# Kernel optimization log

Hardware: AMD Instinct MI355X
Metric: run time of the kernel (lower is better)

Reference implementation:

```python
import jax, jax.numpy as jnp
import numpy as np

N = 50000   # nodes
E = 600000  # directed edges (self-loops added inside reference, per GCNConv default)
G = 64      # graphs in the batch
D = 128     # in_features
H = 128     # hidden_channels
C = 10      # num_classes


def setup_inputs() -> dict:
    key = jax.random.key(0)
    ks = jax.random.split(key, 9)
    x = jax.random.normal(ks[0], (N, D), dtype=jnp.float32)
    edge_index = jax.random.randint(ks[1], (2, E), 0, N, dtype=jnp.int64)
    batch = jnp.sort(jax.random.randint(ks[2], (N,), 0, G, dtype=jnp.int64))
    # GCNConv weights (glorot-ish scale) and biases; final linear layer
    W1 = jax.random.normal(ks[3], (D, H), dtype=jnp.float32) / np.sqrt(D).astype(np.float32)
    b1 = jnp.zeros((H,), dtype=jnp.float32)
    W2 = jax.random.normal(ks[4], (H, H), dtype=jnp.float32) / np.sqrt(H).astype(np.float32)
    b2 = jnp.zeros((H,), dtype=jnp.float32)
    Wlin = jax.random.normal(ks[5], (H, C), dtype=jnp.float32) / np.sqrt(H).astype(np.float32)
    blin = jnp.zeros((C,), dtype=jnp.float32)
    return {"x": x, "W1": W1, "b1": b1, "W2": W2, "b2": b2,
            "Wlin": Wlin, "blin": blin, "edge_index": edge_index, "batch": batch}


def _gcn_conv(x, W, b, row, col, norm):
    # x' = D^{-1/2}(A+I)D^{-1/2} (x W) + b ; aggregate messages from row (src) into col (dst)
    h = x @ W                                   # [N, H] dense GEMM
    msg = norm[:, None] * h[row]                # gather by source index [E+N, H]
    out = jax.ops.segment_sum(msg, col, num_segments=N)  # scatter-add to targets
    return out + b


def reference(x, W1, b1, W2, b2, Wlin, blin, edge_index, batch):
    loops = jnp.arange(N, dtype=edge_index.dtype)
    row = jnp.concatenate([edge_index[0], loops])   # sources (+ self loops)
    col = jnp.concatenate([edge_index[1], loops])   # targets (+ self loops)
    # symmetric degree normalization (degrees >= 1 thanks to self loops)
    deg = jax.ops.segment_sum(jnp.ones_like(col, dtype=jnp.float32), col, num_segments=N)
    dinv = jax.lax.rsqrt(deg)
    norm = dinv[row] * dinv[col]                    # [E+N]

    h = jax.nn.relu(_gcn_conv(x, W1, b1, row, col, norm))
    h = _gcn_conv(h, W2, b2, row, col, norm)

    # global mean pool over graphs
    sums = jax.ops.segment_sum(h, batch, num_segments=G)                       # [G, H]
    cnt = jax.ops.segment_sum(jnp.ones((N,), dtype=jnp.float32), batch, num_segments=G)
    pooled = sums / jnp.maximum(cnt, 1.0)[:, None]

    return pooled @ Wlin + blin                     # logits [G, C]
```

## Files before the change

### kernel.cpp

```cpp
#include <hip/hip_runtime.h>

#define NN 50000
#define NE 600000
#define NG 64
#define DIM 128
#define NCLS 10
#define SB 196
#define NNP 50176
#define KBLK 224
#define KCH 224
#define CAP 64
#define E2B ((NE / 2 + 255) / 256)

typedef unsigned short ushort;
typedef __attribute__((ext_vector_type(8))) short short8;
typedef __attribute__((ext_vector_type(4))) float float4v;

__device__ __forceinline__ ushort f2bf(float f) {
    unsigned u = __float_as_uint(f);
    u += 0x7fff + ((u >> 16) & 1);
    return (ushort)(u >> 16);
}
__device__ __forceinline__ void acc8(float* a, uint4 v) {
    a[0] += __uint_as_float(v.x << 16); a[1] += __uint_as_float(v.x & 0xffff0000u);
    a[2] += __uint_as_float(v.y << 16); a[3] += __uint_as_float(v.y & 0xffff0000u);
    a[4] += __uint_as_float(v.z << 16); a[5] += __uint_as_float(v.z & 0xffff0000u);
    a[6] += __uint_as_float(v.w << 16); a[7] += __uint_as_float(v.w & 0xffff0000u);
}

__global__ void k_init(int* __restrict__ cnt, const float* __restrict__ W1,
                       ushort* __restrict__ Wsw, float* __restrict__ Wd) {
    int b = blockIdx.x, t = threadIdx.x;
    if (b < SB) {
        int i = b * 256 + t;
        if (i < NN) cnt[i] = 0;
    } else if (b < SB + 64) {
        int tid = (b - SB) * 256 + t;
        int j = tid & 7;
        int lane = (tid >> 3) & 63;
        int frag = tid >> 9;
        int nt = frag >> 2, kc = frag & 3;
        int k = kc * 32 + (lane >> 4) * 8 + j;
        int n = nt * 16 + (lane & 15);
        Wsw[tid] = f2bf(W1[k * DIM + n]);
    } else {
        float4* w4 = (float4*)Wd;
        int base = (b - SB - 64) * 256 + t;
#pragma unroll
        for (int i = 0; i < 4; ++i)
            w4[base + i * 200704] = make_float4(0.f, 0.f, 0.f, 0.f);
    }
}

__global__ void k_fill(const int* __restrict__ row, const int* __restrict__ col,
                       int* __restrict__ cnt, int* __restrict__ ell) {
    int e = (blockIdx.x * blockDim.x + threadIdx.x) * 2;
    if (e < NE) {
        int2 r = *(const int2*)(row + e);
        int2 c = *(const int2*)(col + e);
        int p0 = atomicAdd(&cnt[c.x], 1);
        if (p0 < CAP) ell[c.x * CAP + p0] = r.x;
        int p1 = atomicAdd(&cnt[c.y], 1);
        if (p1 < CAP) ell[c.y * CAP + p1] = r.y;
    }
}

__global__ void k_pd(const int* __restrict__ cnt, const int* __restrict__ batch,
                     float* __restrict__ dinv, int2* __restrict__ pdat) {
    int i = blockIdx.x * 256 + threadIdx.x;
    if (i < NN) {
        float d = rsqrtf(1.0f + (float)cnt[i]);
        dinv[i] = d;
        pdat[i] = make_int2(batch[i], __float_as_int(d));
    }
}

__global__ void k_wbuild(const int* __restrict__ row, const int* __restrict__ col,
                         const int2* __restrict__ pdat, const float* __restrict__ dinv,
                         float* __restrict__ Wd) {
    int b = blockIdx.x, t = threadIdx.x;
    if (b < E2B) {
        int e = (b * 256 + t) * 2;
        if (e < NE) {
            int2 r = *(const int2*)(row + e);
            int2 c = *(const int2*)(col + e);
            int2 p0 = pdat[c.x];
            int2 p1 = pdat[c.y];
            atomicAdd(&Wd[(size_t)p0.x * NNP + r.x], __int_as_float(p0.y) * dinv[r.x]);
            atomicAdd(&Wd[(size_t)p1.x * NNP + r.y], __int_as_float(p1.y) * dinv[r.y]);
        }
    } else {
        int n = (b - E2B) * 256 + t;
        if (n < NN) {
            int2 p = pdat[n];
            float d = __int_as_float(p.y);
            atomicAdd(&Wd[(size_t)p.x * NNP + n], d * d);
        }
    }
}

__global__ __launch_bounds__(256) void k_gemm_mfma(const float* __restrict__ Ain,
                                                   const ushort* __restrict__ Wsw,
                                                   const float* __restrict__ dinv,
                                                   ushort* __restrict__ Hs) {
    const int t = threadIdx.x;
    const int wave = t >> 6, lane = t & 63;
    const int m = lane & 15, quad = lane >> 4;
    const int row0 = blockIdx.x * 64 + wave * 16;

    short8 bfrag[8][4];
#pragma unroll
    for (int nt = 0; nt < 8; ++nt)
#pragma unroll
        for (int kc = 0; kc < 4; ++kc)
            bfrag[nt][kc] = *(const short8*)(Wsw + ((nt * 4 + kc) * 64 + lane) * 8);

    float4v acc[8];
#pragma unroll
    for (int nt = 0; nt < 8; ++nt) acc[nt] = (float4v){0.f, 0.f, 0.f, 0.f};

    const int row = row0 + m;
    const int rclamp = row < NN ? row : NN - 1;

#pragma unroll
    for (int kc = 0; kc < 4; ++kc) {
        const float* ap = Ain + (size_t)rclamp * DIM + kc * 32 + quad * 8;
        float4 v0 = *(const float4*)ap;
        float4 v1 = *(const float4*)(ap + 4);
        union { short8 v; ushort u[8]; } tmp;
        tmp.u[0] = f2bf(v0.x); tmp.u[1] = f2bf(v0.y);
        tmp.u[2] = f2bf(v0.z); tmp.u[3] = f2bf(v0.w);
        tmp.u[4] = f2bf(v1.x); tmp.u[5] = f2bf(v1.y);
        tmp.u[6] = f2bf(v1.z); tmp.u[7] = f2bf(v1.w);
        short8 a = tmp.v;
#pragma unroll
        for (int nt = 0; nt < 8; ++nt)
            acc[nt] = __builtin_amdgcn_mfma_f32_16x16x32_bf16(a, bfrag[nt][kc], acc[nt], 0, 0, 0);
    }

#pragma unroll
    for (int reg = 0; reg < 4; ++reg) {
        int r = row0 + quad * 4 + reg;
        if (r < NN) {
            float d = dinv[r];
#pragma unroll
            for (int nt = 0; nt < 8; ++nt)
                Hs[(size_t)r * DIM + nt * 16 + m] = f2bf(d * acc[nt][reg]);
        }
    }
}

__global__ __launch_bounds__(256) void k_gather_ell(const int* __restrict__ ell,
                                                    const int* __restrict__ deg,
                                                    const float* __restrict__ dinv,
                                                    const float* __restrict__ bias,
                                                    const ushort* __restrict__ Hs,
                                                    ushort* __restrict__ out) {
    int gt = blockIdx.x * blockDim.x + threadIdx.x;
    int node = gt >> 4, lane = gt & 15;
    if (node >= NN) return;
    const int* rowp = ell + node * CAP;
    int end = min(deg[node], CAP);
    const size_t off = (size_t)lane * 8;

    float a[8] = {0.f, 0.f, 0.f, 0.f, 0.f, 0.f, 0.f, 0.f};
    acc8(a, *(const uint4*)(Hs + (size_t)node * DIM + off));

    int e = 0;
    for (; e + 8 <= end; e += 8) {
        int r0 = rowp[e], r1 = rowp[e + 1], r2 = rowp[e + 2], r3 = rowp[e + 3];
        int r4 = rowp[e + 4], r5 = rowp[e + 5], r6 = rowp[e + 6], r7 = rowp[e + 7];
        uint4 v0 = *(const uint4*)(Hs + (size_t)r0 * DIM + off);
        uint4 v1 = *(const uint4*)(Hs + (size_t)r1 * DIM + off);
        uint4 v2 = *(const uint4*)(Hs + (size_t)r2 * DIM + off);
        uint4 v3 = *(const uint4*)(Hs + (size_t)r3 * DIM + off);
        uint4 v4 = *(const uint4*)(Hs + (size_t)r4 * DIM + off);
        uint4 v5 = *(const uint4*)(Hs + (size_t)r5 * DIM + off);
        uint4 v6 = *(const uint4*)(Hs + (size_t)r6 * DIM + off);
        uint4 v7 = *(const uint4*)(Hs + (size_t)r7 * DIM + off);
        acc8(a, v0); acc8(a, v1); acc8(a, v2); acc8(a, v3);
        acc8(a, v4); acc8(a, v5); acc8(a, v6); acc8(a, v7);
    }
    for (; e + 4 <= end; e += 4) {
        int r0 = rowp[e], r1 = rowp[e + 1], r2 = rowp[e + 2], r3 = rowp[e + 3];
        uint4 v0 = *(const uint4*)(Hs + (size_t)r0 * DIM + off);
        uint4 v1 = *(const uint4*)(Hs + (size_t)r1 * DIM + off);
        uint4 v2 = *(const uint4*)(Hs + (size_t)r2 * DIM + off);
        uint4 v3 = *(const uint4*)(Hs + (size_t)r3 * DIM + off);
        acc8(a, v0); acc8(a, v1); acc8(a, v2); acc8(a, v3);
    }
    for (; e < end; ++e)
        acc8(a, *(const uint4*)(Hs + (size_t)rowp[e] * DIM + off));

    float d = dinv[node];
    float4 b0 = *(const float4*)(bias + off);
    float4 b1 = *(const float4*)(bias + off + 4);
    a[0] = fmaxf(fmaf(a[0], d, b0.x), 0.f); a[1] = fmaxf(fmaf(a[1], d, b0.y), 0.f);
    a[2] = fmaxf(fmaf(a[2], d, b0.z), 0.f); a[3] = fmaxf(fmaf(a[3], d, b0.w), 0.f);
    a[4] = fmaxf(fmaf(a[4], d, b1.x), 0.f); a[5] = fmaxf(fmaf(a[5], d, b1.y), 0.f);
    a[6] = fmaxf(fmaf(a[6], d, b1.z), 0.f); a[7] = fmaxf(fmaf(a[7], d, b1.w), 0.f);
    uint4 o;
    o.x = (unsigned)f2bf(a[0]) | ((unsigned)f2bf(a[1]) << 16);
    o.y = (unsigned)f2bf(a[2]) | ((unsigned)f2bf(a[3]) << 16);
    o.z = (unsigned)f2bf(a[4]) | ((unsigned)f2bf(a[5]) << 16);
    o.w = (unsigned)f2bf(a[6]) | ((unsigned)f2bf(a[7]) << 16);
    *(uint4*)(out + (size_t)node * DIM + off) = o;
}

__global__ __launch_bounds__(256) void k_pool_gemm(const float* __restrict__ Wd,
                                                   const ushort* __restrict__ A2,
                                                   float* __restrict__ partial) {
    const int t = threadIdx.x;
    const int wave = t >> 6, lane = t & 63;
    const int m = lane & 15, quad = lane >> 4;
    const int g = wave * 16 + m;
    const size_t k0 = (size_t)blockIdx.x * KCH;

    float4v acc[8];
#pragma unroll
    for (int nt = 0; nt < 8; ++nt) acc[nt] = (float4v){0.f, 0.f, 0.f, 0.f};

    for (int ks = 0; ks < KCH; ks += 32) {
        const size_t kb = k0 + ks + quad * 8;
        const float* ap = Wd + (size_t)g * NNP + kb;
        float4 a0 = *(const float4*)ap;
        float4 a1 = *(const float4*)(ap + 4);
        union { short8 v; ushort u[8]; } af;
        af.u[0] = f2bf(a0.x); af.u[1] = f2bf(a0.y);
        af.u[2] = f2bf(a0.z); af.u[3] = f2bf(a0.w);
        af.u[4] = f2bf(a1.x); af.u[5] = f2bf(a1.y);
        af.u[6] = f2bf(a1.z); af.u[7] = f2bf(a1.w);

        const ushort* bbase = A2 + kb * DIM + m;
#pragma unroll
        for (int nt = 0; nt < 8; ++nt) {
            union { short8 v; ushort u[8]; } bf;
            const ushort* bp = bbase + nt * 16;
#pragma unroll
            for (int j = 0; j < 8; ++j) bf.u[j] = bp[(size_t)j * DIM];
            acc[nt] = __builtin_amdgcn_mfma_f32_16x16x32_bf16(af.v, bf.v, acc[nt], 0, 0, 0);
        }
    }

    float* dst = partial + (size_t)blockIdx.x * (NG * DIM);
#pragma unroll
    for (int reg = 0; reg < 4; ++reg) {
        int gg = wave * 16 + quad * 4 + reg;
#pragma unroll
        for (int nt = 0; nt < 8; ++nt)
            dst[gg * DIM + nt * 16 + m] = acc[nt][reg];
    }
}

__global__ __launch_bounds__(128) void k_final(const float* __restrict__ partial,
                                               const float* __restrict__ W2,
                                               const float* __restrict__ b2,
                                               const float* __restrict__ Wlin,
                                               const float* __restrict__ blin,
                                               const int* __restrict__ batch,
                                               float* __restrict__ out) {
    const int g = blockIdx.x;
    const int t = threadIdx.x;
    int start;
    { int a = 0, b = NN; while (a < b) { int m = (a + b) >> 1; if (batch[m] < g) a = m + 1; else b = m; } start = a; }
    int end;
    { int a = 0, b = NN; while (a < b) { int m = (a + b) >> 1; if (batch[m] < g + 1) a = m + 1; else b = m; } end = a; }
    const int cnt = end - start;

    float s = 0.f;
    for (int b = 0; b < KBLK; b += 4) {
        float s0 = partial[(size_t)(b + 0) * (NG * DIM) + g * DIM + t];
        float s1 = partial[(size_t)(b + 1) * (NG * DIM) + g * DIM + t];
        float s2 = partial[(size_t)(b + 2) * (NG * DIM) + g * DIM + t];
        float s3 = partial[(size_t)(b + 3) * (NG * DIM) + g * DIM + t];
        s += (s0 + s1) + (s2 + s3);
    }
    __shared__ float P[DIM];
    P[t] = s;
    __syncthreads();
    float acc = 0.f;
    for (int k = 0; k < DIM; ++k) acc += P[k] * W2[k * DIM + t];
    __shared__ float pooled[DIM];
    pooled[t] = (cnt > 0) ? (acc / (float)cnt + b2[t]) : 0.f;
    __syncthreads();
    if (t < NCLS) {
        float s2 = blin[t];
        for (int k = 0; k < DIM; ++k) s2 += pooled[k] * Wlin[k * NCLS + t];
        out[g * NCLS + t] = s2;
    }
}

extern "C" void kernel_launch(void* const* d_in, const int* in_sizes, int n_in,
                              void* d_out, int out_size, void* d_ws, size_t ws_size,
                              hipStream_t stream) {
    const float* x    = (const float*)d_in[0];
    const float* W1   = (const float*)d_in[1];
    const float* b1   = (const float*)d_in[2];
    const float* W2   = (const float*)d_in[3];
    const float* b2   = (const float*)d_in[4];
    const float* Wlin = (const float*)d_in[5];
    const float* blin = (const float*)d_in[6];
    const int* eidx   = (const int*)d_in[7];
    const int* batch  = (const int*)d_in[8];
    float* out = (float*)d_out;

    char* ws = (char*)d_ws;
    int*    cnt   = (int*)(ws + 0);
    float*  dinv  = (float*)(ws + 200000);
    int2*   pdat  = (int2*)(ws + 400000);
    int*    ell   = (int*)(ws + 800000);
    ushort* Wsw   = (ushort*)(ws + 13600000);
    float*  Wd    = (float*)(ws + 13632768);
    ushort* bufA  = (ushort*)(ws + 26477824);
    ushort* bufB  = (ushort*)(ws + 39277824);
    float*  poolpt= (float*)(ws + 52122880);

    const int* erow = eidx;
    const int* ecol = eidx + NE;

    k_init<<<SB + 64 + 784, 256, 0, stream>>>(cnt, W1, Wsw, Wd);
    k_fill<<<E2B, 256, 0, stream>>>(erow, ecol, cnt, ell);
    k_pd<<<SB, 256, 0, stream>>>(cnt, batch, dinv, pdat);

    const int gemm_grid = (NN + 63) / 64;
    const int node_grid = (NN * 16 + 255) / 256;

    k_gemm_mfma<<<gemm_grid, 256, 0, stream>>>(x, Wsw, dinv, bufA);
    k_gather_ell<<<node_grid, 256, 0, stream>>>(ell, cnt, dinv, b1, bufA, bufB);

    k_wbuild<<<E2B + SB, 256, 0, stream>>>(erow, ecol, pdat, dinv, Wd);
    k_pool_gemm<<<KBLK, 256, 0, stream>>>(Wd, bufB, poolpt);

    k_final<<<NG, 128, 0, stream>>>(poolpt, W2, b2, Wlin, blin, batch, out);
}
```

Before: 225.1 us.

## Store first-layer features as fp8 and fold degree normalization into GEMM

The first-layer transformed features are now stored as fp8 (e4m3) instead of bf16. This halves the bytes each neighbor gather in the aggregation kernel reads, and the values are decoded with the hardware packed fp8-to-f32 conversion. The separate degree-normalization kernel and its packed batch/dinv array are removed. dinv is now computed inside the GEMM epilogue, and the gather recomputes it from the clamped degree. This trades accuracy (fp8 mantissa) for bandwidth and removes one launch.

```diff
diff --git a/kernel.cpp b/kernel.cpp
--- a/kernel.cpp
+++ b/kernel.cpp
@@ -13,19 +13,27 @@
 #define E2B ((NE / 2 + 255) / 256)
 
 typedef unsigned short ushort;
+typedef unsigned char uchar;
 typedef __attribute__((ext_vector_type(8))) short short8;
 typedef __attribute__((ext_vector_type(4))) float float4v;
+typedef __attribute__((ext_vector_type(2))) float float2v;
 
 __device__ __forceinline__ ushort f2bf(float f) {
     unsigned u = __float_as_uint(f);
     u += 0x7fff + ((u >> 16) & 1);
     return (ushort)(u >> 16);
 }
-__device__ __forceinline__ void acc8(float* a, uint4 v) {
-    a[0] += __uint_as_float(v.x << 16); a[1] += __uint_as_float(v.x & 0xffff0000u);
-    a[2] += __uint_as_float(v.y << 16); a[3] += __uint_as_float(v.y & 0xffff0000u);
-    a[4] += __uint_as_float(v.z << 16); a[5] += __uint_as_float(v.z & 0xffff0000u);
-    a[6] += __uint_as_float(v.w << 16); a[7] += __uint_as_float(v.w & 0xffff0000u);
+__device__ __forceinline__ uchar f2fp8(float f) {
+    int p = __builtin_amdgcn_cvt_pk_fp8_f32(f, f, 0, false);
+    return (uchar)(p & 0xff);
+}
+__device__ __forceinline__ void accfp8(float* a, uint2 v) {
+    float2v p0 = __builtin_amdgcn_cvt_pk_f32_fp8(v.x, false);
+    float2v p1 = __builtin_amdgcn_cvt_pk_f32_fp8(v.x, true);
+    float2v p2 = __builtin_amdgcn_cvt_pk_f32_fp8(v.y, false);
+    float2v p3 = __builtin_amdgcn_cvt_pk_f32_fp8(v.y, true);
+    a[0] += p0[0]; a[1] += p0[1]; a[2] += p1[0]; a[3] += p1[1];
+    a[4] += p2[0]; a[5] += p2[1]; a[6] += p3[0]; a[7] += p3[1];
 }
 
 __global__ void k_init(int* __restrict__ cnt, const float* __restrict__ W1,
@@ -65,44 +73,11 @@
     }
 }
 
-__global__ void k_pd(const int* __restrict__ cnt, const int* __restrict__ batch,
-                     float* __restrict__ dinv, int2* __restrict__ pdat) {
-    int i = blockIdx.x * 256 + threadIdx.x;
-    if (i < NN) {
-        float d = rsqrtf(1.0f + (float)cnt[i]);
-        dinv[i] = d;
-        pdat[i] = make_int2(batch[i], __float_as_int(d));
-    }
-}
-
-__global__ void k_wbuild(const int* __restrict__ row, const int* __restrict__ col,
-                         const int2* __restrict__ pdat, const float* __restrict__ dinv,
-                         float* __restrict__ Wd) {
-    int b = blockIdx.x, t = threadIdx.x;
-    if (b < E2B) {
-        int e = (b * 256 + t) * 2;
-        if (e < NE) {
-            int2 r = *(const int2*)(row + e);
-            int2 c = *(const int2*)(col + e);
-            int2 p0 = pdat[c.x];
-            int2 p1 = pdat[c.y];
-            atomicAdd(&Wd[(size_t)p0.x * NNP + r.x], __int_as_float(p0.y) * dinv[r.x]);
-            atomicAdd(&Wd[(size_t)p1.x * NNP + r.y], __int_as_float(p1.y) * dinv[r.y]);
-        }
-    } else {
-        int n = (b - E2B) * 256 + t;
-        if (n < NN) {
-            int2 p = pdat[n];
-            float d = __int_as_float(p.y);
-            atomicAdd(&Wd[(size_t)p.x * NNP + n], d * d);
-        }
-    }
-}
-
 __global__ __launch_bounds__(256) void k_gemm_mfma(const float* __restrict__ Ain,
                                                    const ushort* __restrict__ Wsw,
-                                                   const float* __restrict__ dinv,
-                                                   ushort* __restrict__ Hs) {
+                                                   const int* __restrict__ cnt,
+                                                   uchar* __restrict__ Hs,
+                                                   float* __restrict__ dinv) {
     const int t = threadIdx.x;
     const int wave = t >> 6, lane = t & 63;
     const int m = lane & 15, quad = lane >> 4;
@@ -142,19 +117,19 @@
     for (int reg = 0; reg < 4; ++reg) {
         int r = row0 + quad * 4 + reg;
         if (r < NN) {
-            float d = dinv[r];
+            float d = rsqrtf(1.0f + (float)cnt[r]);
+            if (m == 0) dinv[r] = d;
 #pragma unroll
             for (int nt = 0; nt < 8; ++nt)
-                Hs[(size_t)r * DIM + nt * 16 + m] = f2bf(d * acc[nt][reg]);
+                Hs[(size_t)r * DIM + nt * 16 + m] = f2fp8(d * acc[nt][reg]);
         }
     }
 }
 
 __global__ __launch_bounds__(256) void k_gather_ell(const int* __restrict__ ell,
                                                     const int* __restrict__ deg,
-                                                    const float* __restrict__ dinv,
                                                     const float* __restrict__ bias,
-                                                    const ushort* __restrict__ Hs,
+                                                    const uchar* __restrict__ Hs,
                                                     ushort* __restrict__ out) {
     int gt = blockIdx.x * blockDim.x + threadIdx.x;
     int node = gt >> 4, lane = gt & 15;
@@ -164,35 +139,35 @@
     const size_t off = (size_t)lane * 8;
 
     float a[8] = {0.f, 0.f, 0.f, 0.f, 0.f, 0.f, 0.f, 0.f};
-    acc8(a, *(const uint4*)(Hs + (size_t)node * DIM + off));
+    accfp8(a, *(const uint2*)(Hs + (size_t)node * DIM + off));
 
     int e = 0;
     for (; e + 8 <= end; e += 8) {
         int r0 = rowp[e], r1 = rowp[e + 1], r2 = rowp[e + 2], r3 = rowp[e + 3];
         int r4 = rowp[e + 4], r5 = rowp[e + 5], r6 = rowp[e + 6], r7 = rowp[e + 7];
-        uint4 v0 = *(const uint4*)(Hs + (size_t)r0 * DIM + off);
-        uint4 v1 = *(const uint4*)(Hs + (size_t)r1 * DIM + off);
-        uint4 v2 = *(const uint4*)(Hs + (size_t)r2 * DIM + off);
-        uint4 v3 = *(const uint4*)(Hs + (size_t)r3 * DIM + off);
-        uint4 v4 = *(const uint4*)(Hs + (size_t)r4 * DIM + off);
-        uint4 v5 = *(const uint4*)(Hs + (size_t)r5 * DIM + off);
-        uint4 v6 = *(const uint4*)(Hs + (size_t)r6 * DIM + off);
-        uint4 v7 = *(const uint4*)(Hs + (size_t)r7 * DIM + off);
-        acc8(a, v0); acc8(a, v1); acc8(a, v2); acc8(a, v3);
-        acc8(a, v4); acc8(a, v5); acc8(a, v6); acc8(a, v7);
+        uint2 v0 = *(const uint2*)(Hs + (size_t)r0 * DIM + off);
+        uint2 v1 = *(const uint2*)(Hs + (size_t)r1 * DIM + off);
+        uint2 v2 = *(const uint2*)(Hs + (size_t)r2 * DIM + off);
+        uint2 v3 = *(const uint2*)(Hs + (size_t)r3 * DIM + off);
+        uint2 v4 = *(const uint2*)(Hs + (size_t)r4 * DIM + off);
+        uint2 v5 = *(const uint2*)(Hs + (size_t)r5 * DIM + off);
+        uint2 v6 = *(const uint2*)(Hs + (size_t)r6 * DIM + off);
+        uint2 v7 = *(const uint2*)(Hs + (size_t)r7 * DIM + off);
+        accfp8(a, v0); accfp8(a, v1); accfp8(a, v2); accfp8(a, v3);
+        accfp8(a, v4); accfp8(a, v5); accfp8(a, v6); accfp8(a, v7);
     }
     for (; e + 4 <= end; e += 4) {
         int r0 = rowp[e], r1 = rowp[e + 1], r2 = rowp[e + 2], r3 = rowp[e + 3];
-        uint4 v0 = *(const uint4*)(Hs + (size_t)r0 * DIM + off);
-        uint4 v1 = *(const uint4*)(Hs + (size_t)r1 * DIM + off);
-        uint4 v2 = *(const uint4*)(Hs + (size_t)r2 * DIM + off);
-        uint4 v3 = *(const uint4*)(Hs + (size_t)r3 * DIM + off);
-        acc8(a, v0); acc8(a, v1); acc8(a, v2); acc8(a, v3);
+        uint2 v0 = *(const uint2*)(Hs + (size_t)r0 * DIM + off);
+        uint2 v1 = *(const uint2*)(Hs + (size_t)r1 * DIM + off);
+        uint2 v2 = *(const uint2*)(Hs + (size_t)r2 * DIM + off);
+        uint2 v3 = *(const uint2*)(Hs + (size_t)r3 * DIM + off);
+        accfp8(a, v0); accfp8(a, v1); accfp8(a, v2); accfp8(a, v3);
     }
     for (; e < end; ++e)
-        acc8(a, *(const uint4*)(Hs + (size_t)rowp[e] * DIM + off));
-
-    float d = dinv[node];
+        accfp8(a, *(const uint2*)(Hs + (size_t)rowp[e] * DIM + off));
+
+    float d = rsqrtf(1.0f + (float)end);
     float4 b0 = *(const float4*)(bias + off);
     float4 b1 = *(const float4*)(bias + off + 4);
     a[0] = fmaxf(fmaf(a[0], d, b0.x), 0.f); a[1] = fmaxf(fmaf(a[1], d, b0.y), 0.f);
@@ -205,6 +180,27 @@
     o.z = (unsigned)f2bf(a[4]) | ((unsigned)f2bf(a[5]) << 16);
     o.w = (unsigned)f2bf(a[6]) | ((unsigned)f2bf(a[7]) << 16);
     *(uint4*)(out + (size_t)node * DIM + off) = o;
+}
+
+__global__ void k_wbuild(const int* __restrict__ row, const int* __restrict__ col,
+                         const float* __restrict__ dinv, const int* __restrict__ batch,
+                         float* __restrict__ Wd) {
+    int b = blockIdx.x, t = threadIdx.x;
+    if (b < E2B) {
+        int e = (b * 256 + t) * 2;
+        if (e < NE) {
+            int2 r = *(const int2*)(row + e);
+            int2 c = *(const int2*)(col + e);
+            atomicAdd(&Wd[(size_t)batch[c.x] * NNP + r.x], dinv[c.x] * dinv[r.x]);
+            atomicAdd(&Wd[(size_t)batch[c.y] * NNP + r.y], dinv[c.y] * dinv[r.y]);
+        }
+    } else {
+        int n = (b - E2B) * 256 + t;
+        if (n < NN) {
+            float d = dinv[n];
+            atomicAdd(&Wd[(size_t)batch[n] * NNP + n], d * d);
+        }
+    }
 }
 
 __global__ __launch_bounds__(256) void k_pool_gemm(const float* __restrict__ Wd,
@@ -307,28 +303,26 @@
     char* ws = (char*)d_ws;
     int*    cnt   = (int*)(ws + 0);
     float*  dinv  = (float*)(ws + 200000);
-    int2*   pdat  = (int2*)(ws + 400000);
-    int*    ell   = (int*)(ws + 800000);
-    ushort* Wsw   = (ushort*)(ws + 13600000);
-    float*  Wd    = (float*)(ws + 13632768);
-    ushort* bufA  = (ushort*)(ws + 26477824);
-    ushort* bufB  = (ushort*)(ws + 39277824);
-    float*  poolpt= (float*)(ws + 52122880);
+    int*    ell   = (int*)(ws + 400000);
+    ushort* Wsw   = (ushort*)(ws + 13200000);
+    float*  Wd    = (float*)(ws + 13232768);
+    uchar*  Hs1   = (uchar*)(ws + 26077824);
+    ushort* bufB  = (ushort*)(ws + 32477824);
+    float*  poolpt= (float*)(ws + 45322880);
 
     const int* erow = eidx;
     const int* ecol = eidx + NE;
 
     k_init<<<SB + 64 + 784, 256, 0, stream>>>(cnt, W1, Wsw, Wd);
     k_fill<<<E2B, 256, 0, stream>>>(erow, ecol, cnt, ell);
-    k_pd<<<SB, 256, 0, stream>>>(cnt, batch, dinv, pdat);
 
     const int gemm_grid = (NN + 63) / 64;
     const int node_grid = (NN * 16 + 255) / 256;
 
-    k_gemm_mfma<<<gemm_grid, 256, 0, stream>>>(x, Wsw, dinv, bufA);
-    k_gather_ell<<<node_grid, 256, 0, stream>>>(ell, cnt, dinv, b1, bufA, bufB);
-
-    k_wbuild<<<E2B + SB, 256, 0, stream>>>(erow, ecol, pdat, dinv, Wd);
+    k_gemm_mfma<<<gemm_grid, 256, 0, stream>>>(x, Wsw, cnt, Hs1, dinv);
+    k_gather_ell<<<node_grid, 256, 0, stream>>>(ell, cnt, b1, Hs1, bufB);
+
+    k_wbuild<<<E2B + SB, 256, 0, stream>>>(erow, ecol, dinv, batch, Wd);
     k_pool_gemm<<<KBLK, 256, 0, stream>>>(Wd, bufB, poolpt);
 
     k_final<<<NG, 128, 0, stream>>>(poolpt, W2, b2, Wlin, blin, batch, out);
```

Measured after the change: 210.4 us. 6.5% less time.
